# Kernel optimization log

Measured on AMD Instinct MI355X. Metric: run time of the kernel, lower is better.

Reference implementation:

```python
import jax, jax.numpy as jnp
import numpy as np

B, T, D, C = 128, 256, 1280, 100


def setup_inputs() -> dict:
    key = jax.random.key(0)
    ks = jax.random.split(key, 6)
    s = 1.0 / np.sqrt(D)  # PyTorch GRU init scale
    return {
        "seq": jax.random.normal(ks[0], (B, T, D), dtype=jnp.float32),
        "candidates": jax.random.normal(ks[1], (B, C, D), dtype=jnp.float32),
        "W_ih": jax.random.normal(ks[2], (3 * D, D), dtype=jnp.float32) * s,
        "W_hh": jax.random.normal(ks[3], (3 * D, D), dtype=jnp.float32) * s,
        "b_ih": jax.random.normal(ks[4], (3 * D,), dtype=jnp.float32) * s,
        "b_hh": jax.random.normal(ks[5], (3 * D,), dtype=jnp.float32) * s,
    }


def _gru_final_hidden(seq, W_ih, W_hh, b_ih, b_hh):
    # seq: [B, T, D]. PyTorch gate order: r, z, n.
    H = W_hh.shape[1]
    # Precompute input projections for all timesteps: [T, B, 3H]
    x_proj = jnp.einsum('btd,gd->tbg', seq, W_ih) + b_ih
    h0 = jnp.zeros((seq.shape[0], H), dtype=seq.dtype)

    def step(h, xp):
        gi_r, gi_z, gi_n = jnp.split(xp, 3, axis=-1)
        gh = h @ W_hh.T + b_hh  # [B, 3H]
        gh_r, gh_z, gh_n = jnp.split(gh, 3, axis=-1)
        r = jax.nn.sigmoid(gi_r + gh_r)
        z = jax.nn.sigmoid(gi_z + gh_z)
        n = jnp.tanh(gi_n + r * gh_n)
        h_new = (1.0 - z) * n + z * h
        return h_new, None

    h_last, _ = jax.lax.scan(step, h0, x_proj)
    return h_last  # [B, H]


def reference(seq, candidates, W_ih, W_hh, b_ih, b_hh):
    hidden = _gru_final_hidden(seq, W_ih, W_hh, b_ih, b_hh)  # [B, D]
    # einsum '...bd,bcd->...bc' with hidden [1,B,D] then squeeze(0) -> [B, C]
    scores = jnp.einsum('bd,bcd->bc', hidden, candidates)
    return scores
```

## Files before the change

kernel.cpp:

```cpp
#include <hip/hip_runtime.h>
#include <hip/hip_bf16.h>

typedef _Float16 f16;
typedef _Float16 f16x8 __attribute__((ext_vector_type(8)));
typedef float f32x4 __attribute__((ext_vector_type(4)));

#define B_ 128
#define T_ 256
#define D_ 1280
#define G3_ 3840
#define C_ 100
#define TB_ 32768
#define NBUF 16

#define O_H16  0ull
#define O_SEQB 0ull
#define O_WIH  83886080ull
#define O_WHH  93716480ull
#define O_XP   103546880ull
#define O_H32  355860480ull
#define O_BAR  356515840ull

__global__ void k_convert(const float* __restrict__ seq, const float* __restrict__ wih,
                          const float* __restrict__ whh, f16* __restrict__ seqb,
                          f16* __restrict__ wih16, f16* __restrict__ whh16,
                          unsigned* __restrict__ bar) {
  if (blockIdx.x == 0) {
    for (int j = threadIdx.x; j < 10240; j += 256)
      __hip_atomic_store(bar + j, 0u, __ATOMIC_RELAXED, __HIP_MEMORY_SCOPE_AGENT);
  }
  const long NSEQ = (long)TB_ * (D_ / 8);
  const long NW = (long)G3_ * (D_ / 8);
  const long total = NSEQ + 2 * NW;
  for (long i = (long)blockIdx.x * blockDim.x + threadIdx.x; i < total;
       i += (long)gridDim.x * blockDim.x) {
    const float* src;
    f16* dst;
    if (i < NSEQ) {
      long row = i / (D_ / 8), c = i % (D_ / 8);
      long t = row >> 7, b = row & 127;
      src = seq + ((b * T_ + t) * (long)D_ + c * 8);
      dst = seqb + (row * (long)D_ + c * 8);
    } else if (i < NSEQ + NW) {
      long j = i - NSEQ;
      src = wih + j * 8;
      dst = wih16 + j * 8;
    } else {
      long j = i - NSEQ - NW;
      src = whh + j * 8;
      dst = whh16 + j * 8;
    }
    float4 a = *(const float4*)src, b4 = *(const float4*)(src + 4);
    f16x8 o;
    o[0] = (f16)a.x; o[1] = (f16)a.y; o[2] = (f16)a.z; o[3] = (f16)a.w;
    o[4] = (f16)b4.x; o[5] = (f16)b4.y; o[6] = (f16)b4.z; o[7] = (f16)b4.w;
    *(f16x8*)dst = o;
  }
}

__device__ __forceinline__ void gl_lds16(const f16* g, f16* lds) {
  __builtin_amdgcn_global_load_lds((const __attribute__((address_space(1))) void*)g,
                                   (__attribute__((address_space(3))) void*)lds, 16, 0, 0);
}

__global__ __launch_bounds__(256) void k_xproj(const f16* __restrict__ A, const f16* __restrict__ Bw,
                                               const float* __restrict__ bih, f16* __restrict__ Cout) {
  __shared__ f16 Alds[128 * 32];
  __shared__ f16 Blds[128 * 32];
  int bid = blockIdx.x;
  int sb = bid / 240;
  int wi = bid % 240;
  int bm = sb * 8 + (wi & 7);
  int bn = wi >> 3;
  long brow = (long)bm * 128;
  int bcol = bn * 128;
  int tid = threadIdx.x, w = tid >> 6, l = tid & 63;
  int wm = w & 1, wn = w >> 1;

  f32x4 acc[4][4] = {};

  int sr = w * 32 + (l >> 2);
  int sc = (l & 3) * 8;
  const f16* gA = A + (brow + sr) * (long)D_ + sc;
  const f16* gB = Bw + (long)(bcol + sr) * D_ + sc;
  f16* lAw = Alds + (w * 32) * 32;
  f16* lBw = Blds + (w * 32) * 32;

  int fr = l & 15, fc = (l >> 4) * 8;

  for (int kb = 0; kb < 40; ++kb) {
    const f16* a0 = gA + kb * 32;
    const f16* b0 = gB + kb * 32;
    gl_lds16(a0, lAw);
    gl_lds16(a0 + 16 * D_, lAw + 16 * 32);
    gl_lds16(b0, lBw);
    gl_lds16(b0 + 16 * D_, lBw + 16 * 32);
    __syncthreads();
    f16x8 af[4], bf[4];
#pragma unroll
    for (int mt = 0; mt < 4; ++mt) af[mt] = *(const f16x8*)(Alds + (wm * 64 + mt * 16 + fr) * 32 + fc);
#pragma unroll
    for (int nt = 0; nt < 4; ++nt) bf[nt] = *(const f16x8*)(Blds + (wn * 64 + nt * 16 + fr) * 32 + fc);
#pragma unroll
    for (int mt = 0; mt < 4; ++mt)
#pragma unroll
      for (int nt = 0; nt < 4; ++nt)
        acc[mt][nt] = __builtin_amdgcn_mfma_f32_16x16x32_f16(af[mt], bf[nt], acc[mt][nt], 0, 0, 0);
    __syncthreads();
  }
#pragma unroll
  for (int nt = 0; nt < 4; ++nt) {
    int col = bcol + wn * 64 + nt * 16 + fr;
    int g = col / D_;
    int dcol = col - g * D_;
    int cg = dcol >> 4, c16 = dcol & 15;
    float bv = bih[col];
    f16* base = Cout + (((long)bm * 80 + cg) * 3 + g) * 2048 + c16;
#pragma unroll
    for (int mt = 0; mt < 4; ++mt) {
#pragma unroll
      for (int i = 0; i < 4; ++i) {
        int b = wm * 64 + mt * 16 + (l >> 4) * 4 + i;
        base[b * 16] = (f16)(acc[mt][nt][i] + bv);
      }
    }
  }
}

__global__ __launch_bounds__(512, 1) void k_scan(const f16* __restrict__ whh16,
                                                 const f16* __restrict__ xproj,
                                                 const float* __restrict__ bhh,
                                                 f16* __restrict__ h16, float* __restrict__ h32,
                                                 unsigned* __restrict__ bar) {
  __shared__ float red[8][3][4][257];
  int wg = blockIdx.x;
  int rg = wg & 1, cg = wg >> 1;
  int r0 = rg * 64, d0 = cg * 16;
  int tid = threadIdx.x, w = tid >> 6, l = tid & 63;
  int fr = l & 15, fq = l >> 4;
  int er = tid >> 4, ec = tid & 15;
  unsigned* mycnt = bar + (rg * 16 + (cg & 15)) * 32;

  const f16* wbase = whh16 + (long)(d0 + fr) * D_ + w * 160 + fq * 8;
  f16x8 wf[5][3];
#pragma unroll
  for (int j = 0; j < 5; ++j)
#pragma unroll
    for (int g = 0; g < 3; ++g) {
      wf[j][g] = *(const f16x8*)(wbase + (long)g * (D_ * D_) + j * 32);
      asm volatile("" : "+v"(wf[j][g]));
    }

  if ((tid & 1) == 0) {
#pragma unroll
    for (int hh = 0; hh < 2; ++hh) {
      unsigned* p = (unsigned*)(h16 + (long)(r0 + er + hh * 32) * D_ + d0 + ec);
      __hip_atomic_store(p, 0u, __ATOMIC_RELAXED, __HIP_MEMORY_SCOPE_AGENT);
    }
  }

  float bh0 = bhh[0 * D_ + d0 + ec];
  float bh1 = bhh[1 * D_ + d0 + ec];
  float bh2 = bhh[2 * D_ + d0 + ec];
  float hreg[2] = {0.f, 0.f};

  auto poll = [&](unsigned target) {
    unsigned it = 0;
    for (;;) {
      unsigned v = target;
      if (l < 16)
        v = __hip_atomic_load(bar + (rg * 16 + l) * 32, __ATOMIC_RELAXED, __HIP_MEMORY_SCOPE_AGENT);
      if (__all(v >= target)) break;
      __builtin_amdgcn_s_sleep(1);
      if (++it > 500000u) {
        if (l < 16)
          v = __hip_atomic_fetch_add(bar + (rg * 16 + l) * 32, 0u, __ATOMIC_RELAXED,
                                     __HIP_MEMORY_SCOPE_AGENT);
        if (__all(v >= target)) break;
        it = 0;
      }
    }
  };

  const f16* xbase = xproj + ((long)cg * 3) * 2048 + ec;
#define XADDR(tt, hh, g) (xbase + ((long)(tt)*80 * 3 + (g)) * 2048 + (r0 + er + (hh)*32) * 16)

  f16 xgA[2][3], xgB[2][3];
#pragma unroll
  for (int hh = 0; hh < 2; ++hh)
#pragma unroll
    for (int g = 0; g < 3; ++g) {
      xgA[hh][g] = *XADDR(0, hh, g);
      xgB[hh][g] = *XADDR(1, hh, g);
    }

  __syncthreads();
  if (tid == 0)
    __hip_atomic_fetch_add(mycnt, 1u, __ATOMIC_RELAXED, __HIP_MEMORY_SCOPE_AGENT);
  if (tid < 64) {
    poll(5u);
    if (tid == 0) __builtin_amdgcn_fence(__ATOMIC_ACQUIRE, "agent");
  }
  __syncthreads();

  unsigned tgt = 10u;

  auto step = [&](int t, f16 (&xg)[2][3]) {
    const f16* hc = h16 + (long)(t & (NBUF - 1)) * (B_ * D_);
    const f16* ar0 = hc + (long)(r0 + fr) * D_ + w * 160 + fq * 8;
    f32x4 acc[4][3] = {};
#pragma unroll
    for (int j = 0; j < 5; ++j) {
      f16x8 a[4];
#pragma unroll
      for (int m = 0; m < 4; ++m) a[m] = *(const f16x8*)(ar0 + (long)m * 16 * D_ + j * 32);
#pragma unroll
      for (int m = 0; m < 4; ++m) {
        acc[m][0] = __builtin_amdgcn_mfma_f32_16x16x32_f16(a[m], wf[j][0], acc[m][0], 0, 0, 0);
        acc[m][1] = __builtin_amdgcn_mfma_f32_16x16x32_f16(a[m], wf[j][1], acc[m][1], 0, 0, 0);
        acc[m][2] = __builtin_amdgcn_mfma_f32_16x16x32_f16(a[m], wf[j][2], acc[m][2], 0, 0, 0);
      }
    }
#pragma unroll
    for (int m = 0; m < 4; ++m)
#pragma unroll
      for (int g = 0; g < 3; ++g)
#pragma unroll
        for (int i = 0; i < 4; ++i)
          red[w][g][m][(((fq * 4 + i) * 16) + fr) ^ (fq << 2)] = acc[m][g][i];
    asm volatile("s_waitcnt lgkmcnt(0)" ::: "memory");
    __builtin_amdgcn_sched_barrier(0);
    __builtin_amdgcn_s_barrier();
    asm volatile("" ::: "memory");

    float hnew[2];
#pragma unroll
    for (int hh = 0; hh < 2; ++hh) {
      int row = er + hh * 32;
      int m = row >> 4, r16 = row & 15;
      int pos = ((r16 * 16) + ec) ^ ((r16 >> 2) << 2);
      float s0 = 0.f, s1 = 0.f, s2 = 0.f;
#pragma unroll
      for (int ww = 0; ww < 8; ++ww) {
        s0 += red[ww][0][m][pos];
        s1 += red[ww][1][m][pos];
        s2 += red[ww][2][m][pos];
      }
      float xr = (float)xg[hh][0], xz = (float)xg[hh][1], xn = (float)xg[hh][2];
      float r = 1.f / (1.f + __expf(-(xr + s0 + bh0)));
      float z = 1.f / (1.f + __expf(-(xz + s1 + bh1)));
      float pn = xn + r * (s2 + bh2);
      pn = fminf(fmaxf(pn, -30.f), 30.f);
      float e2 = __expf(-2.f * pn);
      float nn = (1.f - e2) / (1.f + e2);
      hnew[hh] = (1.f - z) * nn + z * hreg[hh];
      hreg[hh] = hnew[hh];
    }
    if (t == T_ - 1) return;

    f16* hn = h16 + (long)((t + 1) & (NBUF - 1)) * (B_ * D_);
#pragma unroll
    for (int hh = 0; hh < 2; ++hh) {
      unsigned short bits = __builtin_bit_cast(unsigned short, (f16)hnew[hh]);
      unsigned other = (unsigned)__shfl_xor((int)bits, 1);
      if ((tid & 1) == 0) {
        unsigned val = (unsigned)bits | (other << 16);
        __hip_atomic_store((unsigned*)(hn + (long)(r0 + er + hh * 32) * D_ + d0 + ec), val,
                           __ATOMIC_RELAXED, __HIP_MEMORY_SCOPE_AGENT);
      }
    }
    __builtin_amdgcn_sched_barrier(0);
    {
      int tp = (t + 2 < T_) ? t + 2 : t;
#pragma unroll
      for (int hh = 0; hh < 2; ++hh)
#pragma unroll
        for (int g = 0; g < 3; ++g)
          xg[hh][g] = *XADDR(tp, hh, g);
    }
    __builtin_amdgcn_sched_barrier(0);
    asm volatile("s_waitcnt vmcnt(6)" ::: "memory");
    __builtin_amdgcn_sched_barrier(0);
    __builtin_amdgcn_s_barrier();

    if (tid == 0)
      __hip_atomic_fetch_add(mycnt, 1u, __ATOMIC_RELAXED, __HIP_MEMORY_SCOPE_AGENT);
    if (tid < 64) {
      poll(tgt);
      if (tid == 0 && (((t + 1) & (NBUF - 1)) == 0))
        __builtin_amdgcn_fence(__ATOMIC_ACQUIRE, "agent");
    }
    tgt += 5u;
    __builtin_amdgcn_s_barrier();
    asm volatile("" ::: "memory");
  };

  for (int t2 = 0; t2 < T_; t2 += 2) {
    step(t2, xgA);
    step(t2 + 1, xgB);
  }
#pragma unroll
  for (int hh = 0; hh < 2; ++hh)
    h32[(long)(r0 + er + hh * 32) * D_ + d0 + ec] = hreg[hh];
#undef XADDR
}

__global__ __launch_bounds__(256) void k_scores(const float* __restrict__ h32,
                                                const float* __restrict__ cand,
                                                float* __restrict__ out) {
  int gw = blockIdx.x * 4 + (threadIdx.x >> 6);
  int l = threadIdx.x & 63;
  int b = gw / C_, c = gw % C_;
  const float* hp = h32 + (long)b * D_;
  const float* cp = cand + ((long)b * C_ + c) * D_;
  float s = 0.f;
#pragma unroll
  for (int q = 0; q < 5; ++q) {
    int d = q * 256 + l * 4;
    float4 hv = *(const float4*)(hp + d);
    float4 cv = *(const float4*)(cp + d);
    s += hv.x * cv.x + hv.y * cv.y + hv.z * cv.z + hv.w * cv.w;
  }
#pragma unroll
  for (int off = 32; off > 0; off >>= 1) s += __shfl_down(s, off);
  if (l == 0) out[(long)b * C_ + c] = s;
}

extern "C" void kernel_launch(void* const* d_in, const int* in_sizes, int n_in, void* d_out,
                              int out_size, void* d_ws, size_t ws_size, hipStream_t stream) {
  const float* seq = (const float*)d_in[0];
  const float* cand = (const float*)d_in[1];
  const float* wih = (const float*)d_in[2];
  const float* whh = (const float*)d_in[3];
  const float* bih = (const float*)d_in[4];
  const float* bhh = (const float*)d_in[5];
  char* ws = (char*)d_ws;
  f16* seqb = (f16*)(ws + O_SEQB);
  f16* wih16 = (f16*)(ws + O_WIH);
  f16* whh16 = (f16*)(ws + O_WHH);
  f16* xp = (f16*)(ws + O_XP);
  f16* h16 = (f16*)(ws + O_H16);
  float* h32 = (float*)(ws + O_H32);
  unsigned* bar = (unsigned*)(ws + O_BAR);

  k_convert<<<2048, 256, 0, stream>>>(seq, wih, whh, seqb, wih16, whh16, bar);
  k_xproj<<<7680, 256, 0, stream>>>(seqb, wih16, bih, xp);
  k_scan<<<160, 512, 0, stream>>>(whh16, xp, bhh, h16, h32, bar);
  k_scores<<<3200, 256, 0, stream>>>(h32, cand, (float*)d_out);
}
```

Baseline: 2.399 ms.

## Warp-specialize GRU scan: 5 MFMA waves plus 3 LDS prefetch waves

Splits the 8 waves of the scan kernel into 5 compute waves, each covering 256 of the K dimension with 8 MFMA chunks, and 3 producer waves. The producer waves stream the precomputed input projections into a 7-step-deep LDS ring using global-to-LDS loads. This is meant to take per-thread xproj register prefetch off the compute path and shrink the cross-wave reduction from 8 to 5 partials. In exchange, each compute wave now runs a longer serial MFMA chain per timestep, which could lengthen the critical path of each recurrent step.

```diff
diff --git a/kernel.cpp b/kernel.cpp
--- a/kernel.cpp
+++ b/kernel.cpp
@@ -132,7 +132,8 @@
                                                  const float* __restrict__ bhh,
                                                  f16* __restrict__ h16, float* __restrict__ h32,
                                                  unsigned* __restrict__ bar) {
-  __shared__ float red[8][3][4][257];
+  __shared__ float red[5][3][4][257];
+  __shared__ f16 ring[8][3072];
   int wg = blockIdx.x;
   int rg = wg & 1, cg = wg >> 1;
   int r0 = rg * 64, d0 = cg * 16;
@@ -140,16 +141,31 @@
   int fr = l & 15, fq = l >> 4;
   int er = tid >> 4, ec = tid & 15;
   unsigned* mycnt = bar + (rg * 16 + (cg & 15)) * 32;
-
-  const f16* wbase = whh16 + (long)(d0 + fr) * D_ + w * 160 + fq * 8;
-  f16x8 wf[5][3];
-#pragma unroll
-  for (int j = 0; j < 5; ++j)
-#pragma unroll
-    for (int g = 0; g < 3; ++g) {
-      wf[j][g] = *(const f16x8*)(wbase + (long)g * (D_ * D_) + j * 32);
-      asm volatile("" : "+v"(wf[j][g]));
-    }
+  const bool isProd = (w >= 5);
+
+  f16x8 wf[8][3];
+  if (!isProd) {
+    const f16* wbase = whh16 + (long)(d0 + fr) * D_ + w * 256 + fq * 8;
+#pragma unroll
+    for (int j = 0; j < 8; ++j)
+#pragma unroll
+      for (int g = 0; g < 3; ++g) {
+        wf[j][g] = *(const f16x8*)(wbase + (long)g * (D_ * D_) + j * 32);
+        asm volatile("" : "+v"(wf[j][g]));
+      }
+  }
+
+  auto stage = [&](int tt) {
+    int tp = tt < T_ ? tt : T_ - 1;
+    int p0 = (w - 5) * 2;
+#pragma unroll
+    for (int pp = 0; pp < 2; ++pp) {
+      int p = p0 + pp;
+      int g = p >> 1, hh = p & 1;
+      const f16* src = xproj + ((((long)tp * 80 + cg) * 3 + g) << 11) + (r0 + hh * 32) * 16 + l * 8;
+      gl_lds16(src, &ring[tt & 7][p * 512]);
+    }
+  };
 
   if ((tid & 1) == 0) {
 #pragma unroll
@@ -182,57 +198,53 @@
     }
   };
 
-  const f16* xbase = xproj + ((long)cg * 3) * 2048 + ec;
-#define XADDR(tt, hh, g) (xbase + ((long)(tt)*80 * 3 + (g)) * 2048 + (r0 + er + (hh)*32) * 16)
-
-  f16 xgA[2][3], xgB[2][3];
-#pragma unroll
-  for (int hh = 0; hh < 2; ++hh)
-#pragma unroll
-    for (int g = 0; g < 3; ++g) {
-      xgA[hh][g] = *XADDR(0, hh, g);
-      xgB[hh][g] = *XADDR(1, hh, g);
-    }
-
-  __syncthreads();
+  if (isProd) {
+#pragma unroll
+    for (int s = 0; s < 7; ++s) stage(s);
+  }
+  asm volatile("s_waitcnt vmcnt(0) lgkmcnt(0)" ::: "memory");
+  __builtin_amdgcn_s_barrier();
   if (tid == 0)
     __hip_atomic_fetch_add(mycnt, 1u, __ATOMIC_RELAXED, __HIP_MEMORY_SCOPE_AGENT);
   if (tid < 64) {
     poll(5u);
     if (tid == 0) __builtin_amdgcn_fence(__ATOMIC_ACQUIRE, "agent");
   }
-  __syncthreads();
+  __builtin_amdgcn_s_barrier();
+  asm volatile("" ::: "memory");
 
   unsigned tgt = 10u;
-
-  auto step = [&](int t, f16 (&xg)[2][3]) {
-    const f16* hc = h16 + (long)(t & (NBUF - 1)) * (B_ * D_);
-    const f16* ar0 = hc + (long)(r0 + fr) * D_ + w * 160 + fq * 8;
+  for (int t = 0; t < T_; ++t) {
     f32x4 acc[4][3] = {};
-#pragma unroll
-    for (int j = 0; j < 5; ++j) {
-      f16x8 a[4];
-#pragma unroll
-      for (int m = 0; m < 4; ++m) a[m] = *(const f16x8*)(ar0 + (long)m * 16 * D_ + j * 32);
-#pragma unroll
-      for (int m = 0; m < 4; ++m) {
-        acc[m][0] = __builtin_amdgcn_mfma_f32_16x16x32_f16(a[m], wf[j][0], acc[m][0], 0, 0, 0);
-        acc[m][1] = __builtin_amdgcn_mfma_f32_16x16x32_f16(a[m], wf[j][1], acc[m][1], 0, 0, 0);
-        acc[m][2] = __builtin_amdgcn_mfma_f32_16x16x32_f16(a[m], wf[j][2], acc[m][2], 0, 0, 0);
-      }
-    }
-#pragma unroll
-    for (int m = 0; m < 4; ++m)
-#pragma unroll
-      for (int g = 0; g < 3; ++g)
-#pragma unroll
-        for (int i = 0; i < 4; ++i)
-          red[w][g][m][(((fq * 4 + i) * 16) + fr) ^ (fq << 2)] = acc[m][g][i];
+    if (!isProd) {
+      const f16* hc = h16 + (long)(t & (NBUF - 1)) * (B_ * D_);
+      const f16* ar0 = hc + (long)(r0 + fr) * D_ + w * 256 + fq * 8;
+#pragma unroll
+      for (int j = 0; j < 8; ++j) {
+        f16x8 a[4];
+#pragma unroll
+        for (int m = 0; m < 4; ++m) a[m] = *(const f16x8*)(ar0 + (long)m * 16 * D_ + j * 32);
+#pragma unroll
+        for (int m = 0; m < 4; ++m) {
+          acc[m][0] = __builtin_amdgcn_mfma_f32_16x16x32_f16(a[m], wf[j][0], acc[m][0], 0, 0, 0);
+          acc[m][1] = __builtin_amdgcn_mfma_f32_16x16x32_f16(a[m], wf[j][1], acc[m][1], 0, 0, 0);
+          acc[m][2] = __builtin_amdgcn_mfma_f32_16x16x32_f16(a[m], wf[j][2], acc[m][2], 0, 0, 0);
+        }
+      }
+#pragma unroll
+      for (int m = 0; m < 4; ++m)
+#pragma unroll
+        for (int g = 0; g < 3; ++g)
+#pragma unroll
+          for (int i = 0; i < 4; ++i)
+            red[w][g][m][(((fq * 4 + i) * 16) + fr) ^ (fq << 2)] = acc[m][g][i];
+    }
     asm volatile("s_waitcnt lgkmcnt(0)" ::: "memory");
     __builtin_amdgcn_sched_barrier(0);
     __builtin_amdgcn_s_barrier();
     asm volatile("" ::: "memory");
 
+    const f16* xs = ring[t & 7];
     float hnew[2];
 #pragma unroll
     for (int hh = 0; hh < 2; ++hh) {
@@ -241,12 +253,14 @@
       int pos = ((r16 * 16) + ec) ^ ((r16 >> 2) << 2);
       float s0 = 0.f, s1 = 0.f, s2 = 0.f;
 #pragma unroll
-      for (int ww = 0; ww < 8; ++ww) {
+      for (int ww = 0; ww < 5; ++ww) {
         s0 += red[ww][0][m][pos];
         s1 += red[ww][1][m][pos];
         s2 += red[ww][2][m][pos];
       }
-      float xr = (float)xg[hh][0], xz = (float)xg[hh][1], xn = (float)xg[hh][2];
+      float xr = (float)xs[(0 * 2 + hh) * 512 + er * 16 + ec];
+      float xz = (float)xs[(1 * 2 + hh) * 512 + er * 16 + ec];
+      float xn = (float)xs[(2 * 2 + hh) * 512 + er * 16 + ec];
       float r = 1.f / (1.f + __expf(-(xr + s0 + bh0)));
       float z = 1.f / (1.f + __expf(-(xz + s1 + bh1)));
       float pn = xn + r * (s2 + bh2);
@@ -256,7 +270,7 @@
       hnew[hh] = (1.f - z) * nn + z * hreg[hh];
       hreg[hh] = hnew[hh];
     }
-    if (t == T_ - 1) return;
+    if (t == T_ - 1) break;
 
     f16* hn = h16 + (long)((t + 1) & (NBUF - 1)) * (B_ * D_);
 #pragma unroll
@@ -270,16 +284,13 @@
       }
     }
     __builtin_amdgcn_sched_barrier(0);
-    {
-      int tp = (t + 2 < T_) ? t + 2 : t;
-#pragma unroll
-      for (int hh = 0; hh < 2; ++hh)
-#pragma unroll
-        for (int g = 0; g < 3; ++g)
-          xg[hh][g] = *XADDR(tp, hh, g);
-    }
-    __builtin_amdgcn_sched_barrier(0);
-    asm volatile("s_waitcnt vmcnt(6)" ::: "memory");
+    if (isProd) {
+      stage(t + 7);
+      __builtin_amdgcn_sched_barrier(0);
+      asm volatile("s_waitcnt vmcnt(2)" ::: "memory");
+    } else {
+      asm volatile("s_waitcnt vmcnt(0)" ::: "memory");
+    }
     __builtin_amdgcn_sched_barrier(0);
     __builtin_amdgcn_s_barrier();
 
@@ -293,16 +304,10 @@
     tgt += 5u;
     __builtin_amdgcn_s_barrier();
     asm volatile("" ::: "memory");
-  };
-
-  for (int t2 = 0; t2 < T_; t2 += 2) {
-    step(t2, xgA);
-    step(t2 + 1, xgB);
   }
 #pragma unroll
   for (int hh = 0; hh < 2; ++hh)
     h32[(long)(r0 + er + hh * 32) * D_ + d0 + ec] = hreg[hh];
-#undef XADDR
 }
 
 __global__ __launch_bounds__(256) void k_scores(const float* __restrict__ h32,
```

Result: slower. 2.620 ms (+9.2%).
